# Optimization experiments

Hardware: AMD Instinct MI355X
Metric: run time of the kernel (lower is better)

## Reference

```python
import jax, jax.numpy as jnp
import numpy as np

B, T, H = 32, 512, 1024
NT, NE = 8, 24          # padded per-sample trigger / entity span counts
C_TAGS = 50             # len(all_triggers_entities)
C = C_TAGS + 2          # + START/STOP for CRF
START, STOP = C_TAGS, C_TAGS + 1
A = 36                  # len(all_arguments)
D = 256                 # MLP hidden


def setup_inputs() -> dict:
    key = jax.random.key(0)
    ks = jax.random.split(key, 16)
    s = 0.02
    enc = jax.random.normal(ks[0], (B, T, H), jnp.float32)
    fc_W1 = jax.random.normal(ks[1], (H, D), jnp.float32) * s
    fc_b1 = jnp.zeros((D,), jnp.float32)
    fc_W2 = jax.random.normal(ks[2], (D, C), jnp.float32) * s
    fc_b2 = jnp.zeros((C,), jnp.float32)
    transitions = jax.random.normal(ks[3], (C, C), jnp.float32) * 0.01
    arg_W1 = jax.random.normal(ks[4], (2 * H, D), jnp.float32) * s
    arg_b1 = jnp.zeros((D,), jnp.float32)
    arg_W2 = jax.random.normal(ks[5], (D, A), jnp.float32) * s
    arg_b2 = jnp.zeros((A,), jnp.float32)
    tags = jax.random.randint(ks[6], (B, T), 0, C_TAGS)
    lengths = jax.random.randint(ks[7], (B,), T // 2, T + 1)
    trig_starts = jax.random.randint(ks[8], (B, NT), 0, T - 17)
    trig_ends = trig_starts + jax.random.randint(ks[9], (B, NT), 1, 17)
    trig_mask = (jnp.arange(NT)[None, :] < jax.random.randint(ks[10], (B, 1), 1, NT + 1)).astype(jnp.int32)
    ent_starts = jax.random.randint(ks[11], (B, NE), 0, T - 17)
    ent_ends = ent_starts + jax.random.randint(ks[12], (B, NE), 1, 17)
    ent_mask = (jnp.arange(NE)[None, :] < jax.random.randint(ks[13], (B, 1), 1, NE + 1)).astype(jnp.int32)
    return dict(encoder_out=enc, fc_W1=fc_W1, fc_b1=fc_b1, fc_W2=fc_W2, fc_b2=fc_b2,
                transitions=transitions, arg_W1=arg_W1, arg_b1=arg_b1, arg_W2=arg_W2, arg_b2=arg_b2,
                tags=tags, lengths=lengths,
                trig_starts=trig_starts, trig_ends=trig_ends, trig_mask=trig_mask,
                ent_starts=ent_starts, ent_ends=ent_ends, ent_mask=ent_mask)


def _crf_nll(feats, tags, mask, trans):
    # standard linear-chain CRF negative log likelihood, masked, summed over batch
    maskf = mask.astype(feats.dtype)
    alpha0 = feats[:, 0] + trans[START][None, :]            # [B,C]

    def step(alpha, xs):
        feat_t, m_t = xs                                    # [B,C], [B]
        new = jax.nn.logsumexp(alpha[:, :, None] + trans[None, :, :], axis=1) + feat_t
        return jnp.where(m_t[:, None] > 0, new, alpha), None

    alpha, _ = jax.lax.scan(step, alpha0,
                            (jnp.swapaxes(feats[:, 1:], 0, 1), jnp.swapaxes(mask[:, 1:], 0, 1)))
    logZ = jax.nn.logsumexp(alpha + trans[:, STOP][None, :], axis=1)  # [B]

    emit = jnp.take_along_axis(feats, tags[:, :, None], axis=2)[:, :, 0]
    emit_score = jnp.sum(emit * maskf, axis=1)
    trans_score = jnp.sum(trans[tags[:, :-1], tags[:, 1:]] * maskf[:, 1:], axis=1)
    start_score = trans[START, tags[:, 0]]
    last_idx = jnp.sum(mask, axis=1).astype(jnp.int32) - 1
    last_tag = jnp.take_along_axis(tags, last_idx[:, None], axis=1)[:, 0]
    stop_score = trans[last_tag, STOP]
    gold = emit_score + trans_score + start_score + stop_score
    return jnp.sum(logZ - gold)


def _span_mean(cs, starts, ends):
    # cs: exclusive prefix sums [B,T+1,H]; mean of encoder_out[i, s:e] per span
    s = jnp.take_along_axis(cs, starts[:, :, None], axis=1)
    e = jnp.take_along_axis(cs, ends[:, :, None], axis=1)
    return (e - s) / (ends - starts)[:, :, None].astype(cs.dtype)


def reference(encoder_out, fc_W1, fc_b1, fc_W2, fc_b2, transitions,
              arg_W1, arg_b1, arg_W2, arg_b2,
              tags, lengths, trig_starts, trig_ends, trig_mask,
              ent_starts, ent_ends, ent_mask):
    mask = (jnp.arange(T)[None, :] < lengths[:, None]).astype(jnp.int32)
    # trigger head: Linear -> Dropout(eval=identity) -> Linear (no activation, as in the source)
    feats = (encoder_out @ fc_W1 + fc_b1) @ fc_W2 + fc_b2   # [B,T,C]
    trigger_loss = _crf_nll(feats, tags, mask, transitions)

    # ragged span mean-pooling via prefix sums (replaces the per-sample python loop)
    cs = jnp.concatenate([jnp.zeros((B, 1, H), encoder_out.dtype),
                          jnp.cumsum(encoder_out, axis=1)], axis=1)  # [B,T+1,H]
    trig_vec = _span_mean(cs, trig_starts, trig_ends)       # [B,NT,H]
    ent_vec = _span_mean(cs, ent_starts, ent_ends)          # [B,NE,H]

    # cross product of (trigger, entity) per sample; concat order [entity, trigger]
    ent_b = jnp.broadcast_to(ent_vec[:, None, :, :], (B, NT, NE, H))
    trig_b = jnp.broadcast_to(trig_vec[:, :, None, :], (B, NT, NE, H))
    hidden = jnp.concatenate([ent_b, trig_b], axis=-1).reshape(B * NT * NE, 2 * H)
    logits = (hidden @ arg_W1 + arg_b1) @ arg_W2 + arg_b2   # [B*NT*NE, A]
    pair_mask = (trig_mask[:, :, None] * ent_mask[:, None, :]).reshape(-1).astype(logits.dtype)
    logits = logits * pair_mask[:, None]
    return trigger_loss, logits
```

## Files before the change

kernel.cpp:

```cpp
#include <hip/hip_runtime.h>
#include <math.h>

#define BB 32
#define TT 512
#define HH 1024
#define DD 256
#define CC 52
#define NTT 8
#define NEE 24
#define AA 36
#define STARTT 50
#define STOPP 51
#define NCH 16
#define CL 32

static const size_t OFF_WAT    = 0;
static const size_t OFF_BA     = 73728;
static const size_t OFF_ESTART = 73792;
static const size_t OFF_ESTOP  = 73856;
static const size_t OFF_BEFF   = 73920;
static const size_t OFF_EA     = 73984;
static const size_t OFF_WPACK  = 76032;
static const size_t OFF_FEATS  = 108800;
static const size_t OFF_RMAT   = 2009344;
static const size_t OFF_TVEC   = 4106496;
static const size_t OFF_EVEC   = 4368640;
static const size_t OFF_TLOG   = 5155072;
static const size_t OFF_ELOG   = 5164288;
static const size_t OFF_LOSS   = 5191936;
static const size_t OFF_RED    = 5191968;

typedef __bf16 bf16x8 __attribute__((ext_vector_type(8)));
typedef float f32x4 __attribute__((ext_vector_type(4)));
typedef unsigned int uint4v __attribute__((ext_vector_type(4)));

union U4B { uint4v u; bf16x8 b; };

typedef const __attribute__((address_space(1))) void gvoid_t;
typedef __attribute__((address_space(3))) void lvoid_t;
#define GLOAD16(g, l) __builtin_amdgcn_global_load_lds((gvoid_t*)(g), (lvoid_t*)(l), 16, 0, 0)

static __device__ __forceinline__ unsigned int rne_bf16(float x) {
    unsigned int u = __float_as_uint(x);
    u += 0x7FFFu + ((u >> 16) & 1u);
    return u >> 16;
}

__global__ __launch_bounds__(256) void k1_prep_span(
    const float* __restrict__ enc,
    const float* __restrict__ fc_W1, const float* __restrict__ fc_b1,
    const float* __restrict__ fc_W2, const float* __restrict__ fc_b2,
    const float* __restrict__ trans,
    const float* __restrict__ arg_W1, const float* __restrict__ arg_b1,
    const float* __restrict__ arg_W2, const float* __restrict__ arg_b2,
    const int* __restrict__ ts, const int* __restrict__ te,
    const int* __restrict__ es, const int* __restrict__ ee,
    float* __restrict__ ws)
{
    int bid = blockIdx.x, tid = threadIdx.x;
    if (bid < 128) {
        int g = bid * 256 + tid;
        int s = g >> 2, i = g & 3;
        int kb = s >> 8, nb = (s >> 6) & 3, ln = s & 63;
        int c16 = ln & 15, hi = ln >> 4;
        int n = nb * 16 + c16;
        int k0 = kb * 32 + 8 * hi + 2 * i;
        unsigned int val = 0;
        if (n < CC) {
            const float* w1a = fc_W1 + (size_t)k0 * DD;
            const float* w1b = w1a + DD;
            float a0 = 0.f, a1 = 0.f;
            for (int d = 0; d < DD; ++d) {
                float w2 = fc_W2[d * CC + n];
                a0 = fmaf(w1a[d], w2, a0);
                a1 = fmaf(w1b[d], w2, a1);
            }
            val = rne_bf16(a0) | (rne_bf16(a1) << 16);
        }
        ((unsigned int*)(ws + OFF_WPACK))[g] = val;
    } else if (bid < 416) {
        int f = (bid - 128) * 256 + tid;
        int h = f / 36, a = f - h * 36;
        const float* w1 = arg_W1 + (size_t)h * DD;
        const float* w2 = arg_W2 + a;
        float a0 = 0.f, a1 = 0.f, a2 = 0.f, a3 = 0.f;
        for (int d = 0; d < DD; d += 4) {
            float4 w = *(const float4*)&w1[d];
            a0 = fmaf(w.x, w2[(size_t)(d + 0) * AA], a0);
            a1 = fmaf(w.y, w2[(size_t)(d + 1) * AA], a1);
            a2 = fmaf(w.z, w2[(size_t)(d + 2) * AA], a2);
            a3 = fmaf(w.w, w2[(size_t)(d + 3) * AA], a3);
        }
        ws[OFF_WAT + f] = (a0 + a1) + (a2 + a3);
    } else if (bid < 1440) {
        int sid = bid - 416;
        int b = sid >> 5, s = sid & 31;
        int st, en; float* outv;
        if (s < NTT) {
            st = ts[b * NTT + s]; en = te[b * NTT + s];
            outv = ws + OFF_TVEC + ((size_t)b * NTT + s) * HH;
        } else {
            int e = s - NTT;
            st = es[b * NEE + e]; en = ee[b * NEE + e];
            outv = ws + OFF_EVEC + ((size_t)b * NEE + e) * HH;
        }
        int h4 = tid * 4;
        float ax = 0, ay = 0, az = 0, aw = 0;
        for (int t = st; t < en; ++t) {
            float4 v = *(const float4*)&enc[((size_t)b * TT + t) * HH + h4];
            ax += v.x; ay += v.y; az += v.z; aw += v.w;
        }
        float inv = 1.f / (float)(en - st);
        float4 o; o.x = ax * inv; o.y = ay * inv; o.z = az * inv; o.w = aw * inv;
        *(float4*)&outv[h4] = o;
    } else {
        int f = (bid - 1440) * 256 + tid;
        if (f < 2048) {
            int m = f >> 5, kp = f & 31;
            int k0 = 2 * kp;
            unsigned int wlo = 0, whi = 0;
            if (m < 52) {
                if (k0 < 52)     wlo = rne_bf16(expf(trans[k0 * CC + m]) * 0.015625f);
                if (k0 + 1 < 52) whi = rne_bf16(expf(trans[(k0 + 1) * CC + m]) * 0.015625f);
            }
            ((unsigned int*)(ws + OFF_EA))[f] = wlo | (whi << 16);
        } else if (f < 2112) {
            int j = f - 2048;
            ws[OFF_ESTART + j] = (j < 52) ? expf(trans[STARTT * CC + j]) : 0.f;
        } else if (f < 2176) {
            int j = f - 2112;
            ws[OFF_ESTOP + j] = (j < 52) ? expf(trans[j * CC + STOPP]) : 0.f;
        } else if (f < 2240) {
            int c = f - 2176;
            float acc = 0.f;
            if (c < 52) {
                acc = fc_b2[c];
                for (int d = 0; d < DD; ++d) acc = fmaf(fc_b1[d], fc_W2[d * CC + c], acc);
            }
            ws[OFF_BEFF + c] = acc;
        } else if (f < 2304) {
            int a = f - 2240;
            float acc = 0.f;
            if (a < 36) {
                acc = arg_b2[a];
                for (int d = 0; d < DD; ++d) acc = fmaf(arg_b1[d], arg_W2[d * AA + a], acc);
            }
            ws[OFF_BA + a] = acc;
        } else if (f < 2306) {
            ((unsigned*)(ws + OFF_RED))[f - 2304] = 0u;
        }
    }
}

__global__ __launch_bounds__(256) void k2_fused(
    const float* __restrict__ enc, const int* __restrict__ lengths,
    float* __restrict__ ws)
{
    __shared__ f32x4 Ab[2][512];
    __shared__ uint4v Bb[2][512];
    __shared__ float efsh[32][64];
    int bid = blockIdx.x, tid = threadIdx.x;
    int wid = tid >> 6, lane = tid & 63;
    int c16 = lane & 15, hi = lane >> 4;

    if (bid >= 512) {
        int id = (bid - 512) * 4 + wid;
        int b = id >> 5, s = id & 31;
        int a = lane;
        const float* vec; const float* wt; float* outv; float base;
        if (s < NTT) {
            vec = ws + OFF_TVEC + ((size_t)b * NTT + s) * HH;
            wt  = ws + OFF_WAT + (size_t)1024 * AA;
            outv = ws + OFF_TLOG + ((size_t)b * NTT + s) * AA;
            base = (a < AA) ? ws[OFF_BA + a] : 0.f;
        } else {
            int e = s - NTT;
            vec = ws + OFF_EVEC + ((size_t)b * NEE + e) * HH;
            wt  = ws + OFF_WAT;
            outv = ws + OFF_ELOG + ((size_t)b * NEE + e) * AA;
            base = 0.f;
        }
        if (a < AA) {
            float a0 = 0, a1 = 0, a2 = 0, a3 = 0;
            for (int h = 0; h < HH; h += 4) {
                float4 vv = *(const float4*)&vec[h];
                a0 = fmaf(vv.x, wt[(size_t)(h + 0) * AA + a], a0);
                a1 = fmaf(vv.y, wt[(size_t)(h + 1) * AA + a], a1);
                a2 = fmaf(vv.z, wt[(size_t)(h + 2) * AA + a], a2);
                a3 = fmaf(vv.w, wt[(size_t)(h + 3) * AA + a], a3);
            }
            outv[a] = base + ((a0 + a1) + (a2 + a3));
        }
        return;
    }

    const uint4v* Wpack = (const uint4v*)(ws + OFF_WPACK);
    float* feats = ws + OFF_FEATS;
    int c7 = c16 & 7;
    int row0 = bid * 32;
    int rh = wid & 1;
    int np = wid >> 1;
    int rowL = rh * 16 + c16;

    f32x4 acc[2];
#pragma unroll
    for (int j = 0; j < 2; ++j) {
        float bv = ws[OFF_BEFF + (np * 2 + j) * 16 + c16];
        acc[j][0] = bv; acc[j][1] = bv; acc[j][2] = bv; acc[j][3] = bv;
    }
    {
#pragma unroll
        for (int i = 0; i < 2; ++i) {
            int f = i * 256 + tid;
            int row = f >> 4, qp = f & 15;
            int q = (qp & 8) | ((qp & 7) ^ (row & 7));
            GLOAD16(enc + (size_t)(row0 + row) * HH + q * 4, &Ab[0][i * 256 + wid * 64]);
        }
#pragma unroll
        for (int i = 0; i < 2; ++i) {
            GLOAD16(Wpack + i * 256 + tid, &Bb[0][i * 256 + wid * 64]);
        }
    }
    for (int it = 0; it < 16; ++it) {
        __syncthreads();
        if (it < 15) {
            int buf = (it + 1) & 1;
            int k0 = (it + 1) * 64;
#pragma unroll
            for (int i = 0; i < 2; ++i) {
                int f = i * 256 + tid;
                int row = f >> 4, qp = f & 15;
                int q = (qp & 8) | ((qp & 7) ^ (row & 7));
                GLOAD16(enc + (size_t)(row0 + row) * HH + k0 + q * 4, &Ab[buf][i * 256 + wid * 64]);
            }
#pragma unroll
            for (int i = 0; i < 2; ++i) {
                GLOAD16(Wpack + (size_t)(it + 1) * 512 + i * 256 + tid, &Bb[buf][i * 256 + wid * 64]);
            }
        }
        int cb = it & 1;
#pragma unroll
        for (int kbL = 0; kbL < 2; ++kbL) {
            int q0 = (kbL * 8) | ((2 * hi) ^ c7);
            int q1 = q0 ^ 1;
            f32x4 a0 = Ab[cb][rowL * 16 + q0];
            f32x4 a1 = Ab[cb][rowL * 16 + q1];
            f32x4 lo = (c7 & 1) ? a1 : a0;
            f32x4 hf = (c7 & 1) ? a0 : a1;
            unsigned u0, u1, u2, u3;
            asm("v_cvt_pk_bf16_f32 %0, %1, %2" : "=v"(u0) : "v"(lo[0]), "v"(lo[1]));
            asm("v_cvt_pk_bf16_f32 %0, %1, %2" : "=v"(u1) : "v"(lo[2]), "v"(lo[3]));
            asm("v_cvt_pk_bf16_f32 %0, %1, %2" : "=v"(u2) : "v"(hf[0]), "v"(hf[1]));
            asm("v_cvt_pk_bf16_f32 %0, %1, %2" : "=v"(u3) : "v"(hf[2]), "v"(hf[3]));
            U4B A; A.u[0] = u0; A.u[1] = u1; A.u[2] = u2; A.u[3] = u3;
#pragma unroll
            for (int j = 0; j < 2; ++j) {
                int nb = np * 2 + j;
                U4B Bf; Bf.u = Bb[cb][kbL * 256 + nb * 64 + lane];
                acc[j] = __builtin_amdgcn_mfma_f32_16x16x32_bf16(A.b, Bf.b, acc[j], 0, 0, 0);
            }
        }
    }
#pragma unroll
    for (int j = 0; j < 2; ++j) {
        int col = (np * 2 + j) * 16 + c16;
#pragma unroll
        for (int r = 0; r < 4; ++r) {
            int lrow = rh * 16 + hi * 4 + r;
            float v = acc[j][r];
            float ev = 0.f;
            if (col < CC) {
                feats[(size_t)(row0 + lrow) * CC + col] = v;
                ev = expf(v);
            }
            efsh[lrow][col] = ev;
        }
    }
    __syncthreads();

    int b = bid >> 4, ch = bid & 15;
    int len = lengths[b];
    int tstart = ch * CL + (ch == 0 ? 1 : 0);
    int tend = ch * CL + CL; if (tend > len) tend = len;
    int Le = tend - tstart;
    int nb = wid;
    unsigned int* outm = (unsigned int*)(ws + OFF_RMAT) + (((size_t)b * NCH + ch) << 11);

    if (Le <= 0) {
#pragma unroll
        for (int q = 0; q < 8; ++q) {
            int col0 = nb * 16 + 2 * q;
            unsigned int val = 0;
            if (lane < 52) {
                if (col0 == lane)          val = 0x3F80u;
                else if (col0 + 1 == lane) val = 0x3F800000u;
            }
            outm[lane * 32 + nb * 8 + q] = val;
        }
        return;
    }

    const unsigned short* EA = (const unsigned short*)(ws + OFF_EA);
    bf16x8 Afr[4][2];
#pragma unroll
    for (int mb = 0; mb < 4; ++mb)
#pragma unroll
        for (int kb = 0; kb < 2; ++kb) {
            U4B x; x.u = *(const uint4v*)(EA + (size_t)(mb * 16 + c16) * 64 + kb * 32 + 8 * hi);
            Afr[mb][kb] = x.b;
        }

    unsigned int Bw[2][4];
#pragma unroll
    for (int kb = 0; kb < 2; ++kb)
#pragma unroll
        for (int j = 0; j < 4; ++j) {
            int col = nb * 16 + c16;
            int k0 = kb * 32 + 8 * hi + 2 * j;
            unsigned int v = 0;
            if (col < 52) {
                if (k0 == col)          v = 0x3F80u;
                else if (k0 + 1 == col) v = 0x3F800000u;
            }
            Bw[kb][j] = v;
        }

    unsigned int W[4][2];
    int hsel = hi >> 1;
    int src0 = c16 + 32 * (hi & 1);
    int src1 = src0 + 16;
    int rbase = tstart - ch * CL;

    for (int s = 0; s < Le; ++s) {
        int r = rbase + s;
        U4B b0; b0.u = uint4v{Bw[0][0], Bw[0][1], Bw[0][2], Bw[0][3]};
        U4B b1; b1.u = uint4v{Bw[1][0], Bw[1][1], Bw[1][2], Bw[1][3]};
        f32x4 D[4];
#pragma unroll
        for (int mb = 0; mb < 4; ++mb) {
            f32x4 z = {0.f, 0.f, 0.f, 0.f};
            z = __builtin_amdgcn_mfma_f32_16x16x32_bf16(Afr[mb][0], b0.b, z, 0, 0, 0);
            z = __builtin_amdgcn_mfma_f32_16x16x32_bf16(Afr[mb][1], b1.b, z, 0, 0, 0);
            D[mb] = z;
        }
#pragma unroll
        for (int mb = 0; mb < 4; ++mb) {
            f32x4 cv = *(const f32x4*)&efsh[r][mb * 16 + 4 * hi];
            float d0 = D[mb][0] * cv[0];
            float d1 = D[mb][1] * cv[1];
            float d2 = D[mb][2] * cv[2];
            float d3 = D[mb][3] * cv[3];
            unsigned int w0, w1;
            asm("v_cvt_pk_bf16_f32 %0, %1, %2" : "=v"(w0) : "v"(d0), "v"(d1));
            asm("v_cvt_pk_bf16_f32 %0, %1, %2" : "=v"(w1) : "v"(d2), "v"(d3));
            W[mb][0] = w0; W[mb][1] = w1;
        }
#pragma unroll
        for (int kb = 0; kb < 2; ++kb)
#pragma unroll
            for (int j = 0; j < 4; ++j) {
                int src = (j < 2) ? src0 : src1;
                unsigned int va = (unsigned int)__shfl((int)W[2 * kb][j & 1], src, 64);
                unsigned int vb = (unsigned int)__shfl((int)W[2 * kb + 1][j & 1], src, 64);
                Bw[kb][j] = hsel ? vb : va;
            }
    }

#pragma unroll
    for (int mb = 0; mb < 4; ++mb)
#pragma unroll
        for (int w = 0; w < 2; ++w) {
            unsigned int my = W[mb][w];
            unsigned int ot = (unsigned int)__shfl_xor((int)my, 1, 64);
            unsigned int val;
            int r = 16 * mb + 4 * hi + 2 * w + (c16 & 1);
            if ((c16 & 1) == 0) val = (my & 0xFFFFu) | (ot << 16);
            else                val = (ot >> 16) | (my & 0xFFFF0000u);
            outm[r * 32 + nb * 8 + (c16 >> 1)] = val;
        }
}

__global__ __launch_bounds__(256) void k3_final(
    const float* __restrict__ trans,
    const int* __restrict__ tags, const int* __restrict__ lengths,
    const int* __restrict__ tmask, const int* __restrict__ emask,
    float* __restrict__ ws, float* __restrict__ out)
{
    __shared__ float vsh[64];
    int bid = blockIdx.x, tid = threadIdx.x;
    if (bid >= 32) {
        int idx = (bid - 32) * 256 + tid;
        int a = idx % AA;
        int p = idx / AA;
        int ne = p % NEE;
        int q = p / NEE;
        int nt = q & 7;
        int b = q >> 3;
        float m = (float)(tmask[b * NTT + nt] * emask[b * NEE + ne]);
        out[1 + idx] = (ws[OFF_TLOG + ((size_t)b * NTT + nt) * AA + a] +
                        ws[OFF_ELOG + ((size_t)b * NEE + ne) * AA + a]) * m;
        return;
    }
    if (tid >= 64) return;
    int b = bid, lane = tid;
    int len = lengths[b];
    const unsigned int* Rb = (const unsigned int*)(ws + OFF_RMAT) + ((size_t)b << 15);
    float v = 0.f;
    if (lane < 52) v = ws[OFF_ESTART + lane] * expf(ws[OFF_FEATS + (size_t)b * TT * CC + lane]);
    int S = 0;

    uint4v bf0[8], bf1[8], bf2[8], bf3[8];

#define LOADM(BUF, IDX)                                                        \
    {                                                                          \
        const unsigned int* rr = Rb + (size_t)(IDX) * 2048 + (size_t)lane * 32;\
        _Pragma("unroll")                                                      \
        for (int q = 0; q < 8; ++q) BUF[q] = *(const uint4v*)(rr + q * 4);     \
    }

#define MATVEC(BUF)                                                            \
    {                                                                          \
        vsh[lane] = v;                                                         \
        float c0 = 0, c1 = 0, c2 = 0, c3 = 0;                                  \
        _Pragma("unroll")                                                      \
        for (int q = 0; q < 8; ++q) {                                          \
            uint4v u = BUF[q];                                                 \
            float4 va = *(const float4*)&vsh[q * 8];                           \
            float4 vb = *(const float4*)&vsh[q * 8 + 4];                       \
            c0 = fmaf(__uint_as_float(u[0] << 16), va.x, c0);                  \
            c0 = fmaf(__uint_as_float(u[0] & 0xFFFF0000u), va.y, c0);          \
            c1 = fmaf(__uint_as_float(u[1] << 16), va.z, c1);                  \
            c1 = fmaf(__uint_as_float(u[1] & 0xFFFF0000u), va.w, c1);          \
            c2 = fmaf(__uint_as_float(u[2] << 16), vb.x, c2);                  \
            c2 = fmaf(__uint_as_float(u[2] & 0xFFFF0000u), vb.y, c2);          \
            c3 = fmaf(__uint_as_float(u[3] << 16), vb.z, c3);                  \
            c3 = fmaf(__uint_as_float(u[3] & 0xFFFF0000u), vb.w, c3);          \
        }                                                                      \
        float acc = (c0 + c1) + (c2 + c3);                                     \
        float M = acc;                                                         \
        _Pragma("unroll")                                                      \
        for (int o = 32; o >= 1; o >>= 1) M = fmaxf(M, __shfl_xor(M, o, 64));  \
        int e = (int)((__float_as_uint(M) >> 23) & 0xFF) - 127;                \
        acc *= __uint_as_float((unsigned)(127 - e) << 23);                     \
        S += e; v = acc;                                                       \
    }

    LOADM(bf0, 0) LOADM(bf1, 1) LOADM(bf2, 2) LOADM(bf3, 3)
    MATVEC(bf0)
    LOADM(bf0,  4) MATVEC(bf1)
    LOADM(bf1,  5) MATVEC(bf2)
    LOADM(bf2,  6) MATVEC(bf3)
    LOADM(bf3,  7) MATVEC(bf0)
    LOADM(bf0,  8) MATVEC(bf1)
    LOADM(bf1,  9) MATVEC(bf2)
    LOADM(bf2, 10) MATVEC(bf3)
    LOADM(bf3, 11) MATVEC(bf0)
    LOADM(bf0, 12) MATVEC(bf1)
    LOADM(bf1, 13) MATVEC(bf2)
    LOADM(bf2, 14) MATVEC(bf3)
    LOADM(bf3, 15) MATVEC(bf0)
    MATVEC(bf1)
    MATVEC(bf2)
    MATVEC(bf3)
#undef LOADM
#undef MATVEC

    float z = (lane < 52) ? v * ws[OFF_ESTOP + lane] : 0.f;
#pragma unroll
    for (int o = 32; o >= 1; o >>= 1) z += __shfl_xor(z, o, 64);
    float logZ = logf(z) + (float)(S + 6 * (len - 1)) * 0.6931471805599453f;

    const int* tg = tags + (size_t)b * TT;
    const float* fb = ws + OFF_FEATS + (size_t)b * TT * CC;
    float g = 0.f;
    for (int t = lane; t < TT; t += 64) {
        if (t < len) {
            int ct = tg[t];
            g += fb[(size_t)t * CC + ct];
            if (t + 1 < len) g += trans[ct * CC + tg[t + 1]];
        }
    }
#pragma unroll
    for (int o = 32; o >= 1; o >>= 1) g += __shfl_xor(g, o, 64);

    unsigned old = 0;
    if (lane == 0) {
        g += trans[STARTT * CC + tg[0]] + trans[tg[len - 1] * CC + STOPP];
        ws[OFF_LOSS + b] = logZ - g;
        __threadfence();
        unsigned* lcnt = (unsigned*)(ws + OFF_RED);
        old = __hip_atomic_fetch_add(lcnt, 1u, __ATOMIC_ACQ_REL, __HIP_MEMORY_SCOPE_AGENT);
    }
    old = (unsigned)__shfl((int)old, 0, 64);
    if (old == BB - 1) {
        __threadfence();
        float tv = (lane < BB) ? ((volatile float*)(ws + OFF_LOSS))[lane] : 0.f;
#pragma unroll
        for (int o = 32; o >= 1; o >>= 1) tv += __shfl_xor(tv, o, 64);
        if (lane == 0) out[0] = tv;
    }
}

extern "C" void kernel_launch(void* const* d_in, const int* in_sizes, int n_in,
                              void* d_out, int out_size, void* d_ws, size_t ws_size,
                              hipStream_t stream)
{
    const float* enc    = (const float*)d_in[0];
    const float* fc_W1  = (const float*)d_in[1];
    const float* fc_b1  = (const float*)d_in[2];
    const float* fc_W2  = (const float*)d_in[3];
    const float* fc_b2  = (const float*)d_in[4];
    const float* trans  = (const float*)d_in[5];
    const float* arg_W1 = (const float*)d_in[6];
    const float* arg_b1 = (const float*)d_in[7];
    const float* arg_W2 = (const float*)d_in[8];
    const float* arg_b2 = (const float*)d_in[9];
    const int* tags     = (const int*)d_in[10];
    const int* lengths  = (const int*)d_in[11];
    const int* tstarts  = (const int*)d_in[12];
    const int* tends    = (const int*)d_in[13];
    const int* tmask    = (const int*)d_in[14];
    const int* estarts  = (const int*)d_in[15];
    const int* eends    = (const int*)d_in[16];
    const int* emask    = (const int*)d_in[17];
    float* out = (float*)d_out;
    float* ws  = (float*)d_ws;

    hipLaunchKernelGGL(k1_prep_span, dim3(1450), dim3(256), 0, stream,
                       enc, fc_W1, fc_b1, fc_W2, fc_b2, trans,
                       arg_W1, arg_b1, arg_W2, arg_b2,
                       tstarts, tends, estarts, eends, ws);
    hipLaunchKernelGGL(k2_fused, dim3(768), dim3(256), 0, stream,
                       enc, lengths, ws);
    hipLaunchKernelGGL(k3_final, dim3(896), dim3(256), 0, stream,
                       trans, tags, lengths, tmask, emask, ws, out);
}
```

Measured before the change: 84.56 us.

## Halve CRF chunk length to double k2 blocks and lengthen k3 chain

```diff
diff --git a/kernel.cpp b/kernel.cpp
--- a/kernel.cpp
+++ b/kernel.cpp
@@ -11,8 +11,8 @@
 #define AA 36
 #define STARTT 50
 #define STOPP 51
-#define NCH 16
-#define CL 32
+#define NCH 32
+#define CL 16
 
 static const size_t OFF_WAT    = 0;
 static const size_t OFF_BA     = 73728;
@@ -156,15 +156,15 @@
     const float* __restrict__ enc, const int* __restrict__ lengths,
     float* __restrict__ ws)
 {
-    __shared__ f32x4 Ab[2][512];
+    __shared__ f32x4 Ab[2][256];
     __shared__ uint4v Bb[2][512];
-    __shared__ float efsh[32][64];
+    __shared__ float efsh[16][68];
     int bid = blockIdx.x, tid = threadIdx.x;
     int wid = tid >> 6, lane = tid & 63;
     int c16 = lane & 15, hi = lane >> 4;
 
-    if (bid >= 512) {
-        int id = (bid - 512) * 4 + wid;
+    if (bid >= 1024) {
+        int id = (bid - 1024) * 4 + wid;
         int b = id >> 5, s = id & 31;
         int a = lane;
         const float* vec; const float* wt; float* outv; float base;
@@ -197,25 +197,19 @@
     const uint4v* Wpack = (const uint4v*)(ws + OFF_WPACK);
     float* feats = ws + OFF_FEATS;
     int c7 = c16 & 7;
-    int row0 = bid * 32;
-    int rh = wid & 1;
-    int np = wid >> 1;
-    int rowL = rh * 16 + c16;
-
-    f32x4 acc[2];
-#pragma unroll
-    for (int j = 0; j < 2; ++j) {
-        float bv = ws[OFF_BEFF + (np * 2 + j) * 16 + c16];
-        acc[j][0] = bv; acc[j][1] = bv; acc[j][2] = bv; acc[j][3] = bv;
-    }
+    int row0 = bid * 16;
+    int nb = wid;
+    int rowL = c16;
+
+    f32x4 acc;
     {
-#pragma unroll
-        for (int i = 0; i < 2; ++i) {
-            int f = i * 256 + tid;
-            int row = f >> 4, qp = f & 15;
-            int q = (qp & 8) | ((qp & 7) ^ (row & 7));
-            GLOAD16(enc + (size_t)(row0 + row) * HH + q * 4, &Ab[0][i * 256 + wid * 64]);
-        }
+        float bv = ws[OFF_BEFF + nb * 16 + c16];
+        acc[0] = bv; acc[1] = bv; acc[2] = bv; acc[3] = bv;
+    }
+    {
+        int row = tid >> 4, qp = tid & 15;
+        int q = (qp & 8) | ((qp & 7) ^ (row & 7));
+        GLOAD16(enc + (size_t)(row0 + row) * HH + q * 4, &Ab[0][wid * 64]);
 #pragma unroll
         for (int i = 0; i < 2; ++i) {
             GLOAD16(Wpack + i * 256 + tid, &Bb[0][i * 256 + wid * 64]);
@@ -226,13 +220,9 @@
         if (it < 15) {
             int buf = (it + 1) & 1;
             int k0 = (it + 1) * 64;
-#pragma unroll
-            for (int i = 0; i < 2; ++i) {
-                int f = i * 256 + tid;
-                int row = f >> 4, qp = f & 15;
-                int q = (qp & 8) | ((qp & 7) ^ (row & 7));
-                GLOAD16(enc + (size_t)(row0 + row) * HH + k0 + q * 4, &Ab[buf][i * 256 + wid * 64]);
-            }
+            int row = tid >> 4, qp = tid & 15;
+            int q = (qp & 8) | ((qp & 7) ^ (row & 7));
+            GLOAD16(enc + (size_t)(row0 + row) * HH + k0 + q * 4, &Ab[buf][wid * 64]);
 #pragma unroll
             for (int i = 0; i < 2; ++i) {
                 GLOAD16(Wpack + (size_t)(it + 1) * 512 + i * 256 + tid, &Bb[buf][i * 256 + wid * 64]);
@@ -253,21 +243,16 @@
             asm("v_cvt_pk_bf16_f32 %0, %1, %2" : "=v"(u2) : "v"(hf[0]), "v"(hf[1]));
             asm("v_cvt_pk_bf16_f32 %0, %1, %2" : "=v"(u3) : "v"(hf[2]), "v"(hf[3]));
             U4B A; A.u[0] = u0; A.u[1] = u1; A.u[2] = u2; A.u[3] = u3;
-#pragma unroll
-            for (int j = 0; j < 2; ++j) {
-                int nb = np * 2 + j;
-                U4B Bf; Bf.u = Bb[cb][kbL * 256 + nb * 64 + lane];
-                acc[j] = __builtin_amdgcn_mfma_f32_16x16x32_bf16(A.b, Bf.b, acc[j], 0, 0, 0);
-            }
-        }
-    }
-#pragma unroll
-    for (int j = 0; j < 2; ++j) {
-        int col = (np * 2 + j) * 16 + c16;
+            U4B Bf; Bf.u = Bb[cb][kbL * 256 + nb * 64 + lane];
+            acc = __builtin_amdgcn_mfma_f32_16x16x32_bf16(A.b, Bf.b, acc, 0, 0, 0);
+        }
+    }
+    {
+        int col = nb * 16 + c16;
 #pragma unroll
         for (int r = 0; r < 4; ++r) {
-            int lrow = rh * 16 + hi * 4 + r;
-            float v = acc[j][r];
+            int lrow = hi * 4 + r;
+            float v = acc[r];
             float ev = 0.f;
             if (col < CC) {
                 feats[(size_t)(row0 + lrow) * CC + col] = v;
@@ -278,12 +263,11 @@
     }
     __syncthreads();
 
-    int b = bid >> 4, ch = bid & 15;
+    int b = bid >> 5, ch = bid & 31;
     int len = lengths[b];
     int tstart = ch * CL + (ch == 0 ? 1 : 0);
     int tend = ch * CL + CL; if (tend > len) tend = len;
     int Le = tend - tstart;
-    int nb = wid;
     unsigned int* outm = (unsigned int*)(ws + OFF_RMAT) + (((size_t)b * NCH + ch) << 11);
 
     if (Le <= 0) {
@@ -404,7 +388,7 @@
     if (tid >= 64) return;
     int b = bid, lane = tid;
     int len = lengths[b];
-    const unsigned int* Rb = (const unsigned int*)(ws + OFF_RMAT) + ((size_t)b << 15);
+    const unsigned int* Rb = (const unsigned int*)(ws + OFF_RMAT) + ((size_t)b << 16);
     float v = 0.f;
     if (lane < 52) v = ws[OFF_ESTART + lane] * expf(ws[OFF_FEATS + (size_t)b * TT * CC + lane]);
     int S = 0;
@@ -446,19 +430,35 @@
     }
 
     LOADM(bf0, 0) LOADM(bf1, 1) LOADM(bf2, 2) LOADM(bf3, 3)
+    MATVEC(bf0) LOADM(bf0,  4)
+    MATVEC(bf1) LOADM(bf1,  5)
+    MATVEC(bf2) LOADM(bf2,  6)
+    MATVEC(bf3) LOADM(bf3,  7)
+    MATVEC(bf0) LOADM(bf0,  8)
+    MATVEC(bf1) LOADM(bf1,  9)
+    MATVEC(bf2) LOADM(bf2, 10)
+    MATVEC(bf3) LOADM(bf3, 11)
+    MATVEC(bf0) LOADM(bf0, 12)
+    MATVEC(bf1) LOADM(bf1, 13)
+    MATVEC(bf2) LOADM(bf2, 14)
+    MATVEC(bf3) LOADM(bf3, 15)
+    MATVEC(bf0) LOADM(bf0, 16)
+    MATVEC(bf1) LOADM(bf1, 17)
+    MATVEC(bf2) LOADM(bf2, 18)
+    MATVEC(bf3) LOADM(bf3, 19)
+    MATVEC(bf0) LOADM(bf0, 20)
+    MATVEC(bf1) LOADM(bf1, 21)
+    MATVEC(bf2) LOADM(bf2, 22)
+    MATVEC(bf3) LOADM(bf3, 23)
+    MATVEC(bf0) LOADM(bf0, 24)
+    MATVEC(bf1) LOADM(bf1, 25)
+    MATVEC(bf2) LOADM(bf2, 26)
+    MATVEC(bf3) LOADM(bf3, 27)
+    MATVEC(bf0) LOADM(bf0, 28)
+    MATVEC(bf1) LOADM(bf1, 29)
+    MATVEC(bf2) LOADM(bf2, 30)
+    MATVEC(bf3) LOADM(bf3, 31)
     MATVEC(bf0)
-    LOADM(bf0,  4) MATVEC(bf1)
-    LOADM(bf1,  5) MATVEC(bf2)
-    LOADM(bf2,  6) MATVEC(bf3)
-    LOADM(bf3,  7) MATVEC(bf0)
-    LOADM(bf0,  8) MATVEC(bf1)
-    LOADM(bf1,  9) MATVEC(bf2)
-    LOADM(bf2, 10) MATVEC(bf3)
-    LOADM(bf3, 11) MATVEC(bf0)
-    LOADM(bf0, 12) MATVEC(bf1)
-    LOADM(bf1, 13) MATVEC(bf2)
-    LOADM(bf2, 14) MATVEC(bf3)
-    LOADM(bf3, 15) MATVEC(bf0)
     MATVEC(bf1)
     MATVEC(bf2)
     MATVEC(bf3)
@@ -530,7 +530,7 @@
                        enc, fc_W1, fc_b1, fc_W2, fc_b2, trans,
                        arg_W1, arg_b1, arg_W2, arg_b2,
                        tstarts, tends, estarts, eends, ws);
-    hipLaunchKernelGGL(k2_fused, dim3(768), dim3(256), 0, stream,
+    hipLaunchKernelGGL(k2_fused, dim3(1280), dim3(256), 0, stream,
                        enc, lengths, ws);
     hipLaunchKernelGGL(k3_final, dim3(896), dim3(256), 0, stream,
                        trans, tags, lengths, tmask, emask, ws, out);
```

New measurement: 105.5 us. 1.25x slower.

## Move span pooling into k2 and fuse argument logits with output expansion in k3

Applied to the files above, without the earlier changes.

```diff
diff --git a/kernel.cpp b/kernel.cpp
--- a/kernel.cpp
+++ b/kernel.cpp
@@ -25,8 +25,6 @@
 static const size_t OFF_RMAT   = 2009344;
 static const size_t OFF_TVEC   = 4106496;
 static const size_t OFF_EVEC   = 4368640;
-static const size_t OFF_TLOG   = 5155072;
-static const size_t OFF_ELOG   = 5164288;
 static const size_t OFF_LOSS   = 5191936;
 static const size_t OFF_RED    = 5191968;
 
@@ -46,15 +44,12 @@
     return u >> 16;
 }
 
-__global__ __launch_bounds__(256) void k1_prep_span(
-    const float* __restrict__ enc,
+__global__ __launch_bounds__(256) void k1_prep(
     const float* __restrict__ fc_W1, const float* __restrict__ fc_b1,
     const float* __restrict__ fc_W2, const float* __restrict__ fc_b2,
     const float* __restrict__ trans,
     const float* __restrict__ arg_W1, const float* __restrict__ arg_b1,
     const float* __restrict__ arg_W2, const float* __restrict__ arg_b2,
-    const int* __restrict__ ts, const int* __restrict__ te,
-    const int* __restrict__ es, const int* __restrict__ ee,
     float* __restrict__ ws)
 {
     int bid = blockIdx.x, tid = threadIdx.x;
@@ -92,29 +87,8 @@
             a3 = fmaf(w.w, w2[(size_t)(d + 3) * AA], a3);
         }
         ws[OFF_WAT + f] = (a0 + a1) + (a2 + a3);
-    } else if (bid < 1440) {
-        int sid = bid - 416;
-        int b = sid >> 5, s = sid & 31;
-        int st, en; float* outv;
-        if (s < NTT) {
-            st = ts[b * NTT + s]; en = te[b * NTT + s];
-            outv = ws + OFF_TVEC + ((size_t)b * NTT + s) * HH;
-        } else {
-            int e = s - NTT;
-            st = es[b * NEE + e]; en = ee[b * NEE + e];
-            outv = ws + OFF_EVEC + ((size_t)b * NEE + e) * HH;
-        }
-        int h4 = tid * 4;
-        float ax = 0, ay = 0, az = 0, aw = 0;
-        for (int t = st; t < en; ++t) {
-            float4 v = *(const float4*)&enc[((size_t)b * TT + t) * HH + h4];
-            ax += v.x; ay += v.y; az += v.z; aw += v.w;
-        }
-        float inv = 1.f / (float)(en - st);
-        float4 o; o.x = ax * inv; o.y = ay * inv; o.z = az * inv; o.w = aw * inv;
-        *(float4*)&outv[h4] = o;
     } else {
-        int f = (bid - 1440) * 256 + tid;
+        int f = (bid - 416) * 256 + tid;
         if (f < 2048) {
             int m = f >> 5, kp = f & 31;
             int k0 = 2 * kp;
@@ -154,6 +128,8 @@
 
 __global__ __launch_bounds__(256) void k2_fused(
     const float* __restrict__ enc, const int* __restrict__ lengths,
+    const int* __restrict__ ts, const int* __restrict__ te,
+    const int* __restrict__ es, const int* __restrict__ ee,
     float* __restrict__ ws)
 {
     __shared__ f32x4 Ab[2][512];
@@ -164,33 +140,26 @@
     int c16 = lane & 15, hi = lane >> 4;
 
     if (bid >= 512) {
-        int id = (bid - 512) * 4 + wid;
-        int b = id >> 5, s = id & 31;
-        int a = lane;
-        const float* vec; const float* wt; float* outv; float base;
+        int sid = bid - 512;
+        int b = sid >> 5, s = sid & 31;
+        int st, en; float* outv;
         if (s < NTT) {
-            vec = ws + OFF_TVEC + ((size_t)b * NTT + s) * HH;
-            wt  = ws + OFF_WAT + (size_t)1024 * AA;
-            outv = ws + OFF_TLOG + ((size_t)b * NTT + s) * AA;
-            base = (a < AA) ? ws[OFF_BA + a] : 0.f;
+            st = ts[b * NTT + s]; en = te[b * NTT + s];
+            outv = ws + OFF_TVEC + ((size_t)b * NTT + s) * HH;
         } else {
             int e = s - NTT;
-            vec = ws + OFF_EVEC + ((size_t)b * NEE + e) * HH;
-            wt  = ws + OFF_WAT;
-            outv = ws + OFF_ELOG + ((size_t)b * NEE + e) * AA;
-            base = 0.f;
-        }
-        if (a < AA) {
-            float a0 = 0, a1 = 0, a2 = 0, a3 = 0;
-            for (int h = 0; h < HH; h += 4) {
-                float4 vv = *(const float4*)&vec[h];
-                a0 = fmaf(vv.x, wt[(size_t)(h + 0) * AA + a], a0);
-                a1 = fmaf(vv.y, wt[(size_t)(h + 1) * AA + a], a1);
-                a2 = fmaf(vv.z, wt[(size_t)(h + 2) * AA + a], a2);
-                a3 = fmaf(vv.w, wt[(size_t)(h + 3) * AA + a], a3);
-            }
-            outv[a] = base + ((a0 + a1) + (a2 + a3));
-        }
+            st = es[b * NEE + e]; en = ee[b * NEE + e];
+            outv = ws + OFF_EVEC + ((size_t)b * NEE + e) * HH;
+        }
+        int h4 = tid * 4;
+        float ax = 0, ay = 0, az = 0, aw = 0;
+        for (int t = st; t < en; ++t) {
+            float4 v = *(const float4*)&enc[((size_t)b * TT + t) * HH + h4];
+            ax += v.x; ay += v.y; az += v.z; aw += v.w;
+        }
+        float inv = 1.f / (float)(en - st);
+        float4 o; o.x = ax * inv; o.y = ay * inv; o.z = az * inv; o.w = aw * inv;
+        *(float4*)&outv[h4] = o;
         return;
     }
 
@@ -387,40 +356,71 @@
     float* __restrict__ ws, float* __restrict__ out)
 {
     __shared__ float vsh[64];
+    __shared__ float logits_sh[32][40];
     int bid = blockIdx.x, tid = threadIdx.x;
+    int wid = tid >> 6, lane = tid & 63;
+
     if (bid >= 32) {
-        int idx = (bid - 32) * 256 + tid;
-        int a = idx % AA;
-        int p = idx / AA;
-        int ne = p % NEE;
-        int q = p / NEE;
-        int nt = q & 7;
-        int b = q >> 3;
-        float m = (float)(tmask[b * NTT + nt] * emask[b * NEE + ne]);
-        out[1 + idx] = (ws[OFF_TLOG + ((size_t)b * NTT + nt) * AA + a] +
-                        ws[OFF_ELOG + ((size_t)b * NEE + ne) * AA + a]) * m;
+        int b = bid - 32;
+#pragma unroll
+        for (int u = 0; u < 8; ++u) {
+            int s = wid * 8 + u;
+            const float* vec; const float* wt; float base;
+            if (s < NTT) {
+                vec = ws + OFF_TVEC + ((size_t)b * NTT + s) * HH;
+                wt  = ws + OFF_WAT + (size_t)1024 * AA;
+                base = (lane < AA) ? ws[OFF_BA + lane] : 0.f;
+            } else {
+                int e = s - NTT;
+                vec = ws + OFF_EVEC + ((size_t)b * NEE + e) * HH;
+                wt  = ws + OFF_WAT;
+                base = 0.f;
+            }
+            if (lane < AA) {
+                float a0 = 0, a1 = 0, a2 = 0, a3 = 0;
+                for (int h = 0; h < HH; h += 4) {
+                    float4 vv = *(const float4*)&vec[h];
+                    a0 = fmaf(vv.x, wt[(size_t)(h + 0) * AA + lane], a0);
+                    a1 = fmaf(vv.y, wt[(size_t)(h + 1) * AA + lane], a1);
+                    a2 = fmaf(vv.z, wt[(size_t)(h + 2) * AA + lane], a2);
+                    a3 = fmaf(vv.w, wt[(size_t)(h + 3) * AA + lane], a3);
+                }
+                logits_sh[s][lane] = base + ((a0 + a1) + (a2 + a3));
+            }
+        }
+        __syncthreads();
+        for (int u = tid; u < NTT * NEE * AA; u += 256) {
+            int nt = u / (NEE * AA);
+            int rem = u - nt * (NEE * AA);
+            int ne = rem / AA;
+            int a = rem - ne * AA;
+            float m = (float)(tmask[b * NTT + nt] * emask[b * NEE + ne]);
+            out[1 + (((size_t)b * NTT + nt) * NEE + ne) * AA + a] =
+                (logits_sh[nt][a] + logits_sh[NTT + ne][a]) * m;
+        }
         return;
     }
+
     if (tid >= 64) return;
-    int b = bid, lane = tid;
+    int b = bid, lane2 = tid;
     int len = lengths[b];
     const unsigned int* Rb = (const unsigned int*)(ws + OFF_RMAT) + ((size_t)b << 15);
     float v = 0.f;
-    if (lane < 52) v = ws[OFF_ESTART + lane] * expf(ws[OFF_FEATS + (size_t)b * TT * CC + lane]);
+    if (lane2 < 52) v = ws[OFF_ESTART + lane2] * expf(ws[OFF_FEATS + (size_t)b * TT * CC + lane2]);
     int S = 0;
 
     uint4v bf0[8], bf1[8], bf2[8], bf3[8];
 
 #define LOADM(BUF, IDX)                                                        \
     {                                                                          \
-        const unsigned int* rr = Rb + (size_t)(IDX) * 2048 + (size_t)lane * 32;\
+        const unsigned int* rr = Rb + (size_t)(IDX) * 2048 + (size_t)lane2 * 32;\
         _Pragma("unroll")                                                      \
         for (int q = 0; q < 8; ++q) BUF[q] = *(const uint4v*)(rr + q * 4);     \
     }
 
 #define MATVEC(BUF)                                                            \
     {                                                                          \
-        vsh[lane] = v;                                                         \
+        vsh[lane2] = v;                                                        \
         float c0 = 0, c1 = 0, c2 = 0, c3 = 0;                                  \
         _Pragma("unroll")                                                      \
         for (int q = 0; q < 8; ++q) {                                          \
@@ -465,7 +465,7 @@
 #undef LOADM
 #undef MATVEC
 
-    float z = (lane < 52) ? v * ws[OFF_ESTOP + lane] : 0.f;
+    float z = (lane2 < 52) ? v * ws[OFF_ESTOP + lane2] : 0.f;
 #pragma unroll
     for (int o = 32; o >= 1; o >>= 1) z += __shfl_xor(z, o, 64);
     float logZ = logf(z) + (float)(S + 6 * (len - 1)) * 0.6931471805599453f;
@@ -473,7 +473,7 @@
     const int* tg = tags + (size_t)b * TT;
     const float* fb = ws + OFF_FEATS + (size_t)b * TT * CC;
     float g = 0.f;
-    for (int t = lane; t < TT; t += 64) {
+    for (int t = lane2; t < TT; t += 64) {
         if (t < len) {
             int ct = tg[t];
             g += fb[(size_t)t * CC + ct];
@@ -484,7 +484,7 @@
     for (int o = 32; o >= 1; o >>= 1) g += __shfl_xor(g, o, 64);
 
     unsigned old = 0;
-    if (lane == 0) {
+    if (lane2 == 0) {
         g += trans[STARTT * CC + tg[0]] + trans[tg[len - 1] * CC + STOPP];
         ws[OFF_LOSS + b] = logZ - g;
         __threadfence();
@@ -494,10 +494,10 @@
     old = (unsigned)__shfl((int)old, 0, 64);
     if (old == BB - 1) {
         __threadfence();
-        float tv = (lane < BB) ? ((volatile float*)(ws + OFF_LOSS))[lane] : 0.f;
+        float tv = (lane2 < BB) ? ((volatile float*)(ws + OFF_LOSS))[lane2] : 0.f;
 #pragma unroll
         for (int o = 32; o >= 1; o >>= 1) tv += __shfl_xor(tv, o, 64);
-        if (lane == 0) out[0] = tv;
+        if (lane2 == 0) out[0] = tv;
     }
 }
 
@@ -526,12 +526,11 @@
     float* out = (float*)d_out;
     float* ws  = (float*)d_ws;
 
-    hipLaunchKernelGGL(k1_prep_span, dim3(1450), dim3(256), 0, stream,
-                       enc, fc_W1, fc_b1, fc_W2, fc_b2, trans,
-                       arg_W1, arg_b1, arg_W2, arg_b2,
-                       tstarts, tends, estarts, eends, ws);
-    hipLaunchKernelGGL(k2_fused, dim3(768), dim3(256), 0, stream,
-                       enc, lengths, ws);
-    hipLaunchKernelGGL(k3_final, dim3(896), dim3(256), 0, stream,
+    hipLaunchKernelGGL(k1_prep, dim3(426), dim3(256), 0, stream,
+                       fc_W1, fc_b1, fc_W2, fc_b2, trans,
+                       arg_W1, arg_b1, arg_W2, arg_b2, ws);
+    hipLaunchKernelGGL(k2_fused, dim3(1536), dim3(256), 0, stream,
+                       enc, lengths, tstarts, tends, estarts, eends, ws);
+    hipLaunchKernelGGL(k3_final, dim3(64), dim3(256), 0, stream,
                        trans, tags, lengths, tmask, emask, ws, out);
 }
```

Result: slower. 226.3 us (+167.6%).
